# Kernel tuning notes

Measured on AMD Instinct MI355X. Metric: run time of the kernel, lower is better.

Reference implementation:

```python
import jax, jax.numpy as jnp
import numpy as np

D_MODEL, H, D_K, D_V, M = 1024, 8, 128, 128, 16
B, NQ, NK = 8, 1024, 1024


def setup_inputs() -> dict:
    key = jax.random.key(0)
    ks = jax.random.split(key, 12)
    f = jnp.float32
    inp = {
        "queries": jax.random.normal(ks[0], (B, NQ, D_MODEL), f),
        "keys": jax.random.normal(ks[1], (B, NK, D_MODEL), f),
        "values": jax.random.normal(ks[2], (B, NK, D_MODEL), f),
        "attention_mask": jax.random.bernoulli(ks[3], 0.15, (B, H, NQ, NK)),
        # linear weights stored (in, out) so y = x @ W + b
        "Wq": jax.random.normal(ks[4], (D_MODEL, H * D_K), f) * (2.0 / D_MODEL) ** 0.5,
        "bq": jnp.zeros((H * D_K,), f),
        "Wk": jax.random.normal(ks[5], (D_MODEL, H * D_K), f) * (2.0 / D_MODEL) ** 0.5,
        "bk": jnp.zeros((H * D_K,), f),
        "Wv": jax.random.normal(ks[6], (D_MODEL, H * D_V), f) * (2.0 / D_MODEL) ** 0.5,
        "bv": jnp.zeros((H * D_V,), f),
        "Wo": jax.random.normal(ks[7], (H * D_V, D_MODEL), f) * (2.0 / D_MODEL) ** 0.5,
        "bo": jnp.zeros((D_MODEL,), f),
        "m_k": jax.random.normal(ks[8], (1, M, H * D_K), f) * (1.0 / D_K),
        "m_v": jax.random.normal(ks[9], (1, M, H * D_V), f) * (1.0 / M),
    }
    return inp


def reference(queries, keys, values, attention_mask, Wq, bq, Wk, bk, Wv, bv, Wo, bo, m_k, m_v):
    b, nq, _ = queries.shape
    nk = keys.shape[1]
    scale = 1.0 / np.sqrt(D_K).astype(np.float32)

    q = (queries @ Wq + bq).reshape(b, nq, H, D_K)                # (b,nq,h,dk)
    mk = np.sqrt(D_K).astype(np.float32) * jnp.broadcast_to(m_k, (b, M, H * D_K))
    mv = np.sqrt(M).astype(np.float32) * jnp.broadcast_to(m_v, (b, M, H * D_V))
    k = jnp.concatenate([keys @ Wk + bk, mk], axis=1).reshape(b, nk + M, H, D_K)
    v = jnp.concatenate([values @ Wv + bv, mv], axis=1).reshape(b, nk + M, H, D_V)

    att = jnp.einsum("bqhd,bkhd->bhqk", q, k) * scale             # (b,h,nq,nk+m)
    # mask only the real-key slice; memory slots are never masked
    full_mask = jnp.concatenate(
        [attention_mask, jnp.zeros((b, H, nq, M), dtype=bool)], axis=-1)
    att = jnp.where(full_mask, -jnp.inf, att)
    att = jax.nn.softmax(att, axis=-1)

    out = jnp.einsum("bhqk,bkhd->bqhd", att, v).reshape(b, nq, H * D_V)
    out = out @ Wo + bo
    return out, att.reshape(-1, nq, nk)
```

## Files before the change

kernel.cpp:

```cpp
#include <hip/hip_runtime.h>


typedef unsigned short u16;
typedef unsigned int   u32;
typedef _Float16 f16x8 __attribute__((ext_vector_type(8)));
typedef short    s16x8 __attribute__((ext_vector_type(8)));
typedef float    f32x4 __attribute__((ext_vector_type(4)));

#define MFMA_F16(a, b, c) __builtin_amdgcn_mfma_f32_16x16x32_f16((a), (b), (c), 0, 0, 0)

#define NQS    1024
#define NKM    1040
#define KSP    1088
#define MW     34
#define SCALE_QK 0.088388347648318447f

__device__ __forceinline__ u16 f2h(float f) {
  _Float16 h = (_Float16)f;
  return __builtin_bit_cast(u16, h);
}
__device__ __forceinline__ f16x8 ld_h8(const u16* p) {
  s16x8 r = *(const s16x8*)p;
  return __builtin_bit_cast(f16x8, r);
}

__global__ void cvt16_kernel(const float* __restrict__ in, u16* __restrict__ out, int n4) {
  for (int i = blockIdx.x * blockDim.x + threadIdx.x; i < n4;
       i += gridDim.x * blockDim.x) {
    float4 v = ((const float4*)in)[i];
    ushort4 h;
    h.x = f2h(v.x); h.y = f2h(v.y); h.z = f2h(v.z); h.w = f2h(v.w);
    ((ushort4*)out)[i] = h;
  }
}

__global__ __launch_bounds__(256)
void wtrans16_kernel(const float* __restrict__ w, u16* __restrict__ t16) {
  __shared__ float t[64][65];
  const int bx = blockIdx.x & 15;
  const int by = blockIdx.x >> 4;
  const int r = threadIdx.x >> 4, c4 = threadIdx.x & 15;
#pragma unroll
  for (int i = 0; i < 4; ++i) {
    const int row = bx * 64 + r + i * 16;
    float4 v = *(const float4*)&w[row * 1024 + by * 64 + c4 * 4];
    t[r + i * 16][c4 * 4 + 0] = v.x;
    t[r + i * 16][c4 * 4 + 1] = v.y;
    t[r + i * 16][c4 * 4 + 2] = v.z;
    t[r + i * 16][c4 * 4 + 3] = v.w;
  }
  __syncthreads();
  const int l = threadIdx.x & 63, og = threadIdx.x >> 6;
#pragma unroll
  for (int j = 0; j < 16; ++j) {
    const int o_local = og + j * 4;
    t16[(by * 64 + o_local) * 1024 + bx * 64 + l] = f2h(t[l][o_local]);
  }
}

__global__ void mk_fill_kernel(const float* __restrict__ m_k, u16* __restrict__ kh) {
  int idx = blockIdx.x * 256 + threadIdx.x;
  int bh = idx >> 13, ko = (idx >> 7) & 63, dk = idx & 127;
  int h = bh & 7;
  float v = 0.f;
  if (ko < 16) v = 11.313708498984760f * m_k[ko * 1024 + h * 128 + dk];
  kh[((size_t)bh * KSP + 1024 + ko) * 128 + dk] = f2h(v);
}

__global__ void mv_fill_kernel(const float* __restrict__ m_v, u16* __restrict__ vt) {
  int idx = blockIdx.x * 256 + threadIdx.x;
  int bh = idx >> 13, dv = (idx >> 6) & 127, ko = idx & 63;
  int h = bh & 7;
  float v = (ko < 16) ? 4.0f * m_v[ko * 1024 + h * 128 + dv] : 0.f;
  vt[((size_t)bh * 128 + dv) * KSP + 1024 + ko] = f2h(v);
}

__global__ void maskbits_kernel(const int* __restrict__ mask, u32* __restrict__ mbits) {
  const int lane = threadIdx.x & 63;
  const int nwave = (gridDim.x * blockDim.x) >> 6;
  int wid = (blockIdx.x * blockDim.x + threadIdx.x) >> 6;
  for (int g = wid; g < 262144; g += nwave) {
    const int4 m = *(const int4*)&mask[(size_t)g * 256 + lane * 4];
    u32 nib = (m.x ? 1u : 0u) | (m.y ? 2u : 0u) | (m.z ? 4u : 0u) | (m.w ? 8u : 0u);
    u32 v = nib << ((lane & 7) * 4);
    v |= __shfl_xor(v, 1);
    v |= __shfl_xor(v, 2);
    v |= __shfl_xor(v, 4);
    if ((lane & 7) == 0) {
      const int row = g >> 2;
      const int word = ((g & 3) << 3) + (lane >> 3);
      mbits[row * MW + word] = v;
    }
  }
}

__global__ void maskfill_kernel(u32* __restrict__ mbits) {
  int idx = blockIdx.x * 256 + threadIdx.x;
  mbits[idx * MW + 32] = 0xFFFF0000u;
  mbits[idx * MW + 33] = 0xFFFFFFFFu;
}

__device__ __forceinline__ void stage_tile(const u16* __restrict__ gbase,
                                           u16* sbase, int w, int lane) {
#pragma unroll
  for (int i = 0; i < 4; ++i) {
    const u16* src = gbase + (w * 32 + i * 8 + (lane >> 3)) * 1024 + (lane & 7) * 8;
    u16* dst = sbase + (w * 32 + i * 8) * 64;
    __builtin_amdgcn_global_load_lds(
        (const __attribute__((address_space(1))) void*)src,
        (__attribute__((address_space(3))) void*)dst, 16, 0, 0);
  }
}

enum { EPI_Q16 = 0, EPI_K16 = 1, EPI_VT = 2, EPI_OUT = 3 };

template <int EPI>
__global__ __launch_bounds__(256)
void gemm_kernel(const u16* __restrict__ A, const u16* __restrict__ B,
                 const float* __restrict__ bias,
                 u16* __restrict__ oH, float* __restrict__ oF) {
  __shared__ u16 sA[128 * 64];
  __shared__ u16 sB[128 * 64];
  const int lane = threadIdx.x & 63, w = threadIdx.x >> 6;
  const int bn = blockIdx.x & 7, bm = blockIdx.x >> 3;
  const int wr = w >> 1, wc = w & 1;

  f32x4 acc[4][4];
  const f32x4 fz = {0.f, 0.f, 0.f, 0.f};
#pragma unroll
  for (int m = 0; m < 4; ++m)
#pragma unroll
    for (int n = 0; n < 4; ++n) acc[m][n] = fz;

  for (int kt = 0; kt < 16; ++kt) {
    const int kb = kt * 64;
    stage_tile(A + bm * 128 * 1024 + kb, sA, w, lane);
    stage_tile(B + bn * 128 * 1024 + kb, sB, w, lane);
    __syncthreads();
    const int ro = lane & 15;
#pragma unroll
    for (int kk = 0; kk < 2; ++kk) {
      const int co = kk * 32 + (lane >> 4) * 8;
      f16x8 a[4], b[4];
#pragma unroll
      for (int m = 0; m < 4; ++m) a[m] = ld_h8(&sA[(wr * 64 + m * 16 + ro) * 64 + co]);
#pragma unroll
      for (int n = 0; n < 4; ++n) b[n] = ld_h8(&sB[(wc * 64 + n * 16 + ro) * 64 + co]);
#pragma unroll
      for (int m = 0; m < 4; ++m)
#pragma unroll
        for (int n = 0; n < 4; ++n)
          acc[m][n] = MFMA_F16(a[m], b[n], acc[m][n]);
    }
    __syncthreads();
  }

#pragma unroll
  for (int m = 0; m < 4; ++m)
#pragma unroll
    for (int n = 0; n < 4; ++n) {
      const int row0 = bm * 128 + wr * 64 + m * 16 + ((lane >> 4) << 2);
      const int col = bn * 128 + wc * 64 + n * 16 + (lane & 15);
      const float bv = bias[col];
#pragma unroll
      for (int r = 0; r < 4; ++r) {
        const float y = acc[m][n][r] + bv;
        const int row = row0 + r;
        if constexpr (EPI == EPI_Q16) {
          oH[row * 1024 + col] = f2h(y * SCALE_QK);
        } else if constexpr (EPI == EPI_K16) {
          const int b = row >> 10, key = row & 1023;
          oH[((size_t)(b * 8 + (col >> 7)) * KSP + key) * 128 + (col & 127)] = f2h(y);
        } else if constexpr (EPI == EPI_VT) {
          const int b = row >> 10, key = row & 1023;
          oH[((size_t)(b * 8 + (col >> 7)) * 128 + (col & 127)) * KSP + key] = f2h(y);
        } else {
          oF[row * 1024 + col] = y;
        }
      }
    }
}

__global__ __launch_bounds__(256, 3)
void attn_kernel(const u16* __restrict__ qh, const u16* __restrict__ kh,
                 const u16* __restrict__ vt, const u32* __restrict__ mbits,
                 float* __restrict__ att, u16* __restrict__ obuf) {
  __shared__ __align__(16) u16 sK[64 * 128];
  __shared__ __align__(16) u16 sV[128 * 72];
  __shared__ __align__(16) float sAtt[4][16][36];
  const int tid = threadIdx.x;
  const int lane = tid & 63, w = tid >> 6;

  const int d = blockIdx.x;
  const int j = d >> 3;
  const int bh = (d & 7) * 8 + (j >> 4);
  const int qblk = j & 15;
  const int h = bh & 7;
  const int b = bh >> 3;
  const int qrow0 = qblk * 64 + w * 16;
  const int grow0 = b * NQS + qrow0;
  const int ro = lane & 15, go = lane >> 4;

  f16x8 qf[4];
#pragma unroll
  for (int kk = 0; kk < 4; ++kk)
    qf[kk] = ld_h8(&qh[(grow0 + ro) * 1024 + h * 128 + kk * 32 + go * 8]);

  const u16* khb = kh + (size_t)bh * KSP * 128;
  const u16* vtb = vt + (size_t)bh * 128 * KSP;
  const u32* mbb = mbits + (size_t)bh * NQS * MW;
  float* attb = att + (size_t)(bh * NQS + qrow0) * NKM;

  const int r_k  = tid >> 4;
  const int cb_k = (tid & 15) * 16;
  const u16* kp0 = khb + r_k * 128 + (cb_k >> 1);
  const int dk0 = r_k * 256 + (cb_k ^ ((r_k & 7) << 4));
  const int vrow[4] = {(0 * 256 + tid) >> 3, (1 * 256 + tid) >> 3,
                       (2 * 256 + tid) >> 3, (3 * 256 + tid) >> 3};
  const int vc8[4]  = {(0 * 256 + tid) & 7, (1 * 256 + tid) & 7,
                       (2 * 256 + tid) & 7, (3 * 256 + tid) & 7};

  const f32x4 fz = {0.f, 0.f, 0.f, 0.f};
  float lsum[4] = {0.f, 0.f, 0.f, 0.f};

  {
    s16x8 rk0 = *(const s16x8*)(kp0);
    s16x8 rk1 = *(const s16x8*)(kp0 + 16 * 128);
    s16x8 rk2 = *(const s16x8*)(kp0 + 32 * 128);
    s16x8 rk3 = *(const s16x8*)(kp0 + 48 * 128);
    for (int c = 0; c < 17; ++c) {
      __syncthreads();
      *(s16x8*)((char*)sK + dk0)         = rk0;
      *(s16x8*)((char*)sK + dk0 + 4096)  = rk1;
      *(s16x8*)((char*)sK + dk0 + 8192)  = rk2;
      *(s16x8*)((char*)sK + dk0 + 12288) = rk3;
      if (c < 16) {
        const u16* p = kp0 + (c + 1) * 64 * 128;
        rk0 = *(const s16x8*)(p);
        rk1 = *(const s16x8*)(p + 16 * 128);
        rk2 = *(const s16x8*)(p + 32 * 128);
        rk3 = *(const s16x8*)(p + 48 * 128);
      }
      __syncthreads();
      u32 mw0[4], mw1[4];
#pragma unroll
      for (int r = 0; r < 4; ++r) {
        const int row = qrow0 + (go << 2) + r;
        mw0[r] = mbb[row * MW + 2 * c];
        mw1[r] = mbb[row * MW + 2 * c + 1];
      }
#pragma unroll
      for (int t = 0; t < 4; ++t) {
        f32x4 s = fz;
        const int rr = t * 16 + ro;
        const int sw = (rr & 7) << 4;
        __builtin_amdgcn_s_setprio(1);
#pragma unroll
        for (int kk = 0; kk < 4; ++kk) {
          const int off = rr * 256 + ((kk * 64 + go * 16) ^ sw);
          s = MFMA_F16(qf[kk], ld_h8((const u16*)((const char*)sK + off)), s);
        }
        __builtin_amdgcn_s_setprio(0);
        const int bit = (t & 1) * 16 + ro;
#pragma unroll
        for (int r = 0; r < 4; ++r) {
          const u32 mw = (t < 2) ? mw0[r] : mw1[r];
          const bool dead = (mw >> bit) & 1;
          lsum[r] += dead ? 0.f : __expf(s[r]);
        }
      }
    }
  }

  float inv[4];
#pragma unroll
  for (int r = 0; r < 4; ++r) {
    lsum[r] += __shfl_xor(lsum[r], 1);
    lsum[r] += __shfl_xor(lsum[r], 2);
    lsum[r] += __shfl_xor(lsum[r], 4);
    lsum[r] += __shfl_xor(lsum[r], 8);
    inv[r] = 1.0f / lsum[r];
  }

  f32x4 oacc[8];
#pragma unroll
  for (int n = 0; n < 8; ++n) oacc[n] = fz;

  s16x8 rk0 = *(const s16x8*)(kp0);
  s16x8 rk1 = *(const s16x8*)(kp0 + 16 * 128);
  s16x8 rk2 = *(const s16x8*)(kp0 + 32 * 128);
  s16x8 rk3 = *(const s16x8*)(kp0 + 48 * 128);
  s16x8 rv0 = *(const s16x8*)(vtb + (size_t)vrow[0] * KSP + vc8[0] * 8);
  s16x8 rv1 = *(const s16x8*)(vtb + (size_t)vrow[1] * KSP + vc8[1] * 8);
  s16x8 rv2 = *(const s16x8*)(vtb + (size_t)vrow[2] * KSP + vc8[2] * 8);
  s16x8 rv3 = *(const s16x8*)(vtb + (size_t)vrow[3] * KSP + vc8[3] * 8);

  for (int c = 0; c < 17; ++c) {
    __syncthreads();
    *(s16x8*)((char*)sK + dk0)         = rk0;
    *(s16x8*)((char*)sK + dk0 + 4096)  = rk1;
    *(s16x8*)((char*)sK + dk0 + 8192)  = rk2;
    *(s16x8*)((char*)sK + dk0 + 12288) = rk3;
    *(s16x8*)((char*)sV + vrow[0] * 144 + vc8[0] * 16) = rv0;
    *(s16x8*)((char*)sV + vrow[1] * 144 + vc8[1] * 16) = rv1;
    *(s16x8*)((char*)sV + vrow[2] * 144 + vc8[2] * 16) = rv2;
    *(s16x8*)((char*)sV + vrow[3] * 144 + vc8[3] * 16) = rv3;
    if (c < 16) {
      const int nkb = (c + 1) * 64;
      const u16* p = kp0 + nkb * 128;
      rk0 = *(const s16x8*)(p);
      rk1 = *(const s16x8*)(p + 16 * 128);
      rk2 = *(const s16x8*)(p + 32 * 128);
      rk3 = *(const s16x8*)(p + 48 * 128);
      rv0 = *(const s16x8*)(vtb + (size_t)vrow[0] * KSP + nkb + vc8[0] * 8);
      rv1 = *(const s16x8*)(vtb + (size_t)vrow[1] * KSP + nkb + vc8[1] * 8);
      rv2 = *(const s16x8*)(vtb + (size_t)vrow[2] * KSP + nkb + vc8[2] * 8);
      rv3 = *(const s16x8*)(vtb + (size_t)vrow[3] * KSP + nkb + vc8[3] * 8);
    }
    __syncthreads();

    u32 mwc[2][4];
#pragma unroll
    for (int r = 0; r < 4; ++r) {
      const int row = qrow0 + (go << 2) + r;
      mwc[0][r] = mbb[row * MW + 2 * c];
      mwc[1][r] = mbb[row * MW + 2 * c + 1];
    }

#pragma unroll
    for (int t2 = 0; t2 < 2; ++t2) {
#pragma unroll
      for (int t = 0; t < 2; ++t) {
        f32x4 s = fz;
        const int rr = t2 * 32 + t * 16 + ro;
        const int sw = (rr & 7) << 4;
        __builtin_amdgcn_s_setprio(1);
#pragma unroll
        for (int kk = 0; kk < 4; ++kk) {
          const int off = rr * 256 + ((kk * 64 + go * 16) ^ sw);
          s = MFMA_F16(qf[kk], ld_h8((const u16*)((const char*)sK + off)), s);
        }
        __builtin_amdgcn_s_setprio(0);
        const int bit = t * 16 + ro;
#pragma unroll
        for (int r = 0; r < 4; ++r) {
          const int lrow = (go << 2) + r;
          const bool dead = (mwc[t2][r] >> bit) & 1;
          const float e = dead ? 0.f : __expf(s[r]);
          sAtt[w][lrow][t * 16 + ro] = e * inv[r];
        }
      }

      {
        const int kbh = c * 64 + t2 * 32;
        const int arow = lane >> 2, cg = lane & 3;
        if (kbh + cg * 8 < NKM) {
          f32x4 v0 = *(const f32x4*)&sAtt[w][arow][cg * 8];
          f32x4 v1 = *(const f32x4*)&sAtt[w][arow][cg * 8 + 4];
          float* dst = attb + (size_t)arow * NKM + kbh + cg * 8;
          *(f32x4*)dst = v0;
          *(f32x4*)(dst + 4) = v1;
        }
      }

      {
        f32x4 p0 = *(const f32x4*)&sAtt[w][ro][go * 8];
        f32x4 p1 = *(const f32x4*)&sAtt[w][ro][go * 8 + 4];
        f16x8 pa;
        pa[0] = (_Float16)p0[0]; pa[1] = (_Float16)p0[1];
        pa[2] = (_Float16)p0[2]; pa[3] = (_Float16)p0[3];
        pa[4] = (_Float16)p1[0]; pa[5] = (_Float16)p1[1];
        pa[6] = (_Float16)p1[2]; pa[7] = (_Float16)p1[3];
        __builtin_amdgcn_s_setprio(1);
#pragma unroll
        for (int n = 0; n < 8; ++n) {
          f16x8 vb = ld_h8((const u16*)((const char*)sV + (n * 16 + ro) * 144 + t2 * 64 + go * 16));
          oacc[n] = MFMA_F16(pa, vb, oacc[n]);
        }
        __builtin_amdgcn_s_setprio(0);
      }
    }
  }

  __syncthreads();
  {
    u16* os = (u16*)((char*)sK + w * 4096);
#pragma unroll
    for (int n = 0; n < 8; ++n)
#pragma unroll
      for (int r = 0; r < 4; ++r)
        os[((go << 2) + r) * 128 + n * 16 + ro] = f2h(oacc[n][r]);
#pragma unroll
    for (int i = 0; i < 4; ++i) {
      const int idx = i * 64 + lane;
      const int row = idx >> 4, c16 = idx & 15;
      s16x8 v = *(const s16x8*)(os + row * 128 + c16 * 8);
      *(s16x8*)&obuf[(size_t)(grow0 + row) * 1024 + h * 128 + c16 * 8] = v;
    }
  }
}

extern "C" void kernel_launch(void* const* d_in, const int* in_sizes, int n_in,
                              void* d_out, int out_size, void* d_ws, size_t ws_size,
                              hipStream_t stream) {
  const float* queries = (const float*)d_in[0];
  const float* keys    = (const float*)d_in[1];
  const float* values  = (const float*)d_in[2];
  const int*   mask    = (const int*)d_in[3];
  const float* Wq = (const float*)d_in[4];
  const float* bq = (const float*)d_in[5];
  const float* Wk = (const float*)d_in[6];
  const float* bk = (const float*)d_in[7];
  const float* Wv = (const float*)d_in[8];
  const float* bv = (const float*)d_in[9];
  const float* Wo = (const float*)d_in[10];
  const float* bo = (const float*)d_in[11];
  const float* m_k = (const float*)d_in[12];
  const float* m_v = (const float*)d_in[13];

  if (ws_size < 136839168) return;

  char* ws = (char*)d_ws;
  u16* xq  = (u16*)(ws + 0);
  u16* xk  = (u16*)(ws + 16777216);
  u16* xv  = (u16*)(ws + 33554432);
  u16* wq  = (u16*)(ws + 50331648);
  u16* wk  = (u16*)(ws + 52428800);
  u16* wv  = (u16*)(ws + 54525952);
  u16* wo  = (u16*)(ws + 56623104);
  u16* q16 = (u16*)(ws + 58720256);
  u16* k16 = (u16*)(ws + 75497472);
  u16* vt  = (u16*)(ws + 93323264);
  u16* obuf= (u16*)(ws + 111149056);
  u32* mbits=(u32*)(ws + 127926272);

  float* out = (float*)d_out;
  float* att = out + 8388608;

  cvt16_kernel<<<2048, 256, 0, stream>>>(queries, xq, 2097152);
  cvt16_kernel<<<2048, 256, 0, stream>>>(keys,    xk, 2097152);
  cvt16_kernel<<<2048, 256, 0, stream>>>(values,  xv, 2097152);
  wtrans16_kernel<<<256, 256, 0, stream>>>(Wq, wq);
  wtrans16_kernel<<<256, 256, 0, stream>>>(Wk, wk);
  wtrans16_kernel<<<256, 256, 0, stream>>>(Wv, wv);
  wtrans16_kernel<<<256, 256, 0, stream>>>(Wo, wo);
  gemm_kernel<EPI_Q16><<<512, 256, 0, stream>>>(xq, wq, bq, q16, nullptr);
  gemm_kernel<EPI_K16><<<512, 256, 0, stream>>>(xk, wk, bk, k16, nullptr);
  gemm_kernel<EPI_VT> <<<512, 256, 0, stream>>>(xv, wv, bv, vt,  nullptr);
  maskbits_kernel<<<2048, 256, 0, stream>>>(mask, mbits);
  maskfill_kernel<<<256, 256, 0, stream>>>(mbits);
  mk_fill_kernel<<<2048, 256, 0, stream>>>(m_k, k16);
  mv_fill_kernel<<<2048, 256, 0, stream>>>(m_v, vt);
  attn_kernel<<<1024, 256, 0, stream>>>(q16, k16, vt, mbits, att, obuf);
  gemm_kernel<EPI_OUT><<<512, 256, 0, stream>>>(obuf, wo, bo, nullptr, out);
}
```

Before: 415.8 us.

## Batch QKV projections into one launch and store attention probs as fp16 in LDS

The three projection GEMMs are merged into a single 1536-block launch that picks its inputs and epilogue per block, which fills the GPU better and removes two launches. The attention kernel's per-wave probability scratch in LDS changes from fp32 to fp16. This halves LDS use and drops the conversion before the PV MFMA, and launch bounds are raised from 3 to 4 blocks per CU. As a side effect, the attention probabilities written to global memory are now rounded through fp16, which loses precision in that output.

```diff
diff --git a/kernel.cpp b/kernel.cpp
--- a/kernel.cpp
+++ b/kernel.cpp
@@ -112,17 +112,26 @@
   }
 }
 
-enum { EPI_Q16 = 0, EPI_K16 = 1, EPI_VT = 2, EPI_OUT = 3 };
-
-template <int EPI>
 __global__ __launch_bounds__(256)
-void gemm_kernel(const u16* __restrict__ A, const u16* __restrict__ B,
-                 const float* __restrict__ bias,
-                 u16* __restrict__ oH, float* __restrict__ oF) {
+void gemm_proj_kernel(const u16* __restrict__ xq, const u16* __restrict__ xk,
+                      const u16* __restrict__ xv,
+                      const u16* __restrict__ wq, const u16* __restrict__ wk,
+                      const u16* __restrict__ wv,
+                      const float* __restrict__ bq, const float* __restrict__ bk,
+                      const float* __restrict__ bv,
+                      u16* __restrict__ q16, u16* __restrict__ k16,
+                      u16* __restrict__ vt) {
   __shared__ u16 sA[128 * 64];
   __shared__ u16 sB[128 * 64];
   const int lane = threadIdx.x & 63, w = threadIdx.x >> 6;
-  const int bn = blockIdx.x & 7, bm = blockIdx.x >> 3;
+  const int pid = blockIdx.x;
+  const int bn = pid & 7;
+  const int g  = pid >> 3;
+  const int proj = g % 3;
+  const int bm = g / 3;
+  const u16* A = (proj == 0) ? xq : (proj == 1) ? xk : xv;
+  const u16* B = (proj == 0) ? wq : (proj == 1) ? wk : wv;
+  const float* bias = (proj == 0) ? bq : (proj == 1) ? bk : bv;
   const int wr = w >> 1, wc = w & 1;
 
   f32x4 acc[4][4];
@@ -161,33 +170,83 @@
     for (int n = 0; n < 4; ++n) {
       const int row0 = bm * 128 + wr * 64 + m * 16 + ((lane >> 4) << 2);
       const int col = bn * 128 + wc * 64 + n * 16 + (lane & 15);
-      const float bv = bias[col];
+      const float bv_ = bias[col];
 #pragma unroll
       for (int r = 0; r < 4; ++r) {
-        const float y = acc[m][n][r] + bv;
+        const float y = acc[m][n][r] + bv_;
         const int row = row0 + r;
-        if constexpr (EPI == EPI_Q16) {
-          oH[row * 1024 + col] = f2h(y * SCALE_QK);
-        } else if constexpr (EPI == EPI_K16) {
+        if (proj == 0) {
+          q16[row * 1024 + col] = f2h(y * SCALE_QK);
+        } else if (proj == 1) {
           const int b = row >> 10, key = row & 1023;
-          oH[((size_t)(b * 8 + (col >> 7)) * KSP + key) * 128 + (col & 127)] = f2h(y);
-        } else if constexpr (EPI == EPI_VT) {
+          k16[((size_t)(b * 8 + (col >> 7)) * KSP + key) * 128 + (col & 127)] = f2h(y);
+        } else {
           const int b = row >> 10, key = row & 1023;
-          oH[((size_t)(b * 8 + (col >> 7)) * 128 + (col & 127)) * KSP + key] = f2h(y);
-        } else {
-          oF[row * 1024 + col] = y;
-        }
-      }
-    }
-}
-
-__global__ __launch_bounds__(256, 3)
+          vt[((size_t)(b * 8 + (col >> 7)) * 128 + (col & 127)) * KSP + key] = f2h(y);
+        }
+      }
+    }
+}
+
+__global__ __launch_bounds__(256)
+void gemm_out_kernel(const u16* __restrict__ A, const u16* __restrict__ B,
+                     const float* __restrict__ bias, float* __restrict__ oF) {
+  __shared__ u16 sA[128 * 64];
+  __shared__ u16 sB[128 * 64];
+  const int lane = threadIdx.x & 63, w = threadIdx.x >> 6;
+  const int bn = blockIdx.x & 7, bm = blockIdx.x >> 3;
+  const int wr = w >> 1, wc = w & 1;
+
+  f32x4 acc[4][4];
+  const f32x4 fz = {0.f, 0.f, 0.f, 0.f};
+#pragma unroll
+  for (int m = 0; m < 4; ++m)
+#pragma unroll
+    for (int n = 0; n < 4; ++n) acc[m][n] = fz;
+
+  for (int kt = 0; kt < 16; ++kt) {
+    const int kb = kt * 64;
+    stage_tile(A + bm * 128 * 1024 + kb, sA, w, lane);
+    stage_tile(B + bn * 128 * 1024 + kb, sB, w, lane);
+    __syncthreads();
+    const int ro = lane & 15;
+#pragma unroll
+    for (int kk = 0; kk < 2; ++kk) {
+      const int co = kk * 32 + (lane >> 4) * 8;
+      f16x8 a[4], b[4];
+#pragma unroll
+      for (int m = 0; m < 4; ++m) a[m] = ld_h8(&sA[(wr * 64 + m * 16 + ro) * 64 + co]);
+#pragma unroll
+      for (int n = 0; n < 4; ++n) b[n] = ld_h8(&sB[(wc * 64 + n * 16 + ro) * 64 + co]);
+#pragma unroll
+      for (int m = 0; m < 4; ++m)
+#pragma unroll
+        for (int n = 0; n < 4; ++n)
+          acc[m][n] = MFMA_F16(a[m], b[n], acc[m][n]);
+    }
+    __syncthreads();
+  }
+
+#pragma unroll
+  for (int m = 0; m < 4; ++m)
+#pragma unroll
+    for (int n = 0; n < 4; ++n) {
+      const int row0 = bm * 128 + wr * 64 + m * 16 + ((lane >> 4) << 2);
+      const int col = bn * 128 + wc * 64 + n * 16 + (lane & 15);
+      const float bv_ = bias[col];
+#pragma unroll
+      for (int r = 0; r < 4; ++r)
+        oF[(row0 + r) * 1024 + col] = acc[m][n][r] + bv_;
+    }
+}
+
+__global__ __launch_bounds__(256, 4)
 void attn_kernel(const u16* __restrict__ qh, const u16* __restrict__ kh,
                  const u16* __restrict__ vt, const u32* __restrict__ mbits,
                  float* __restrict__ att, u16* __restrict__ obuf) {
   __shared__ __align__(16) u16 sK[64 * 128];
   __shared__ __align__(16) u16 sV[128 * 72];
-  __shared__ __align__(16) float sAtt[4][16][36];
+  __shared__ __align__(16) u16 sAtt[4][16][40];
   const int tid = threadIdx.x;
   const int lane = tid & 63, w = tid >> 6;
 
@@ -347,7 +406,7 @@
           const int lrow = (go << 2) + r;
           const bool dead = (mwc[t2][r] >> bit) & 1;
           const float e = dead ? 0.f : __expf(s[r]);
-          sAtt[w][lrow][t * 16 + ro] = e * inv[r];
+          sAtt[w][lrow][t * 16 + ro] = f2h(e * inv[r]);
         }
       }
 
@@ -355,8 +414,12 @@
         const int kbh = c * 64 + t2 * 32;
         const int arow = lane >> 2, cg = lane & 3;
         if (kbh + cg * 8 < NKM) {
-          f32x4 v0 = *(const f32x4*)&sAtt[w][arow][cg * 8];
-          f32x4 v1 = *(const f32x4*)&sAtt[w][arow][cg * 8 + 4];
+          f16x8 hv = ld_h8(&sAtt[w][arow][cg * 8]);
+          f32x4 v0, v1;
+          v0[0] = (float)hv[0]; v0[1] = (float)hv[1];
+          v0[2] = (float)hv[2]; v0[3] = (float)hv[3];
+          v1[0] = (float)hv[4]; v1[1] = (float)hv[5];
+          v1[2] = (float)hv[6]; v1[3] = (float)hv[7];
           float* dst = attb + (size_t)arow * NKM + kbh + cg * 8;
           *(f32x4*)dst = v0;
           *(f32x4*)(dst + 4) = v1;
@@ -364,13 +427,7 @@
       }
 
       {
-        f32x4 p0 = *(const f32x4*)&sAtt[w][ro][go * 8];
-        f32x4 p1 = *(const f32x4*)&sAtt[w][ro][go * 8 + 4];
-        f16x8 pa;
-        pa[0] = (_Float16)p0[0]; pa[1] = (_Float16)p0[1];
-        pa[2] = (_Float16)p0[2]; pa[3] = (_Float16)p0[3];
-        pa[4] = (_Float16)p1[0]; pa[5] = (_Float16)p1[1];
-        pa[6] = (_Float16)p1[2]; pa[7] = (_Float16)p1[3];
+        f16x8 pa = ld_h8(&sAtt[w][ro][go * 8]);
         __builtin_amdgcn_s_setprio(1);
 #pragma unroll
         for (int n = 0; n < 8; ++n) {
@@ -444,13 +501,12 @@
   wtrans16_kernel<<<256, 256, 0, stream>>>(Wk, wk);
   wtrans16_kernel<<<256, 256, 0, stream>>>(Wv, wv);
   wtrans16_kernel<<<256, 256, 0, stream>>>(Wo, wo);
-  gemm_kernel<EPI_Q16><<<512, 256, 0, stream>>>(xq, wq, bq, q16, nullptr);
-  gemm_kernel<EPI_K16><<<512, 256, 0, stream>>>(xk, wk, bk, k16, nullptr);
-  gemm_kernel<EPI_VT> <<<512, 256, 0, stream>>>(xv, wv, bv, vt,  nullptr);
+  gemm_proj_kernel<<<1536, 256, 0, stream>>>(xq, xk, xv, wq, wk, wv,
+                                             bq, bk, bv, q16, k16, vt);
   maskbits_kernel<<<2048, 256, 0, stream>>>(mask, mbits);
   maskfill_kernel<<<256, 256, 0, stream>>>(mbits);
   mk_fill_kernel<<<2048, 256, 0, stream>>>(m_k, k16);
   mv_fill_kernel<<<2048, 256, 0, stream>>>(m_v, vt);
   attn_kernel<<<1024, 256, 0, stream>>>(q16, k16, vt, mbits, att, obuf);
-  gemm_kernel<EPI_OUT><<<512, 256, 0, stream>>>(obuf, wo, bo, nullptr, out);
-}
+  gemm_out_kernel<<<512, 256, 0, stream>>>(obuf, wo, bo, out);
+}
```

Result: slower. 440.1 us (+5.9%).
